# Optimization experiments

Hardware: AMD Instinct MI355X
Metric: run time of the kernel (lower is better)

The kernel has to match this reference:

```python
import jax, jax.numpy as jnp
import numpy as np

B, T, K, H, HID, OUT = 128, 128, 8, 3, 256, 2
LOG_STD_MIN, LOG_STD_MAX = -20.0, 2.0


def setup_inputs() -> dict:
    key = jax.random.key(0)
    ks = jax.random.split(key, 12)
    def lin(k, fan_in, fan_out, scale=0.05):
        return jax.random.normal(k, (fan_in, fan_out), dtype=jnp.float32) * scale
    return {
        "state": jax.random.normal(ks[0], (B, T, K), dtype=jnp.float32),
        "noise": jax.random.normal(ks[1], (B, T, OUT), dtype=jnp.float32),
        "Wq": lin(ks[2], K, H * K),
        "Wk": lin(ks[3], K, H * K),
        "Wv": lin(ks[4], K, H * K),
        "W1": lin(ks[5], H * K + K, HID),
        "b1": jnp.zeros((HID,), jnp.float32),
        "W2": lin(ks[6], HID, HID),
        "b2": jnp.zeros((HID,), jnp.float32),
        "Wmu": jax.random.uniform(ks[7], (HID, OUT), jnp.float32, -0.003, 0.003),
        "bmu": jax.random.uniform(ks[8], (OUT,), jnp.float32, -0.003, 0.003),
        "Wls": jax.random.uniform(ks[9], (HID, OUT), jnp.float32, -0.003, 0.003),
        "bls": jax.random.uniform(ks[10], (OUT,), jnp.float32, -0.003, 0.003),
    }


def reference(state, noise, Wq, Wk, Wv, W1, b1, W2, b2, Wmu, bmu, Wls, bls):
    b, t, k = state.shape
    h = H
    # off-diagonal gather indices: idx[i, m] = m if m < i else m + 1  (j != i, ascending)
    cols = jnp.arange(t - 1)
    idx = cols[None, :] + (cols[None, :] >= jnp.arange(t)[:, None]).astype(jnp.int32)  # [t, t-1]
    # rel_state[b, i, m] = state[b, idx[i, m]] - state[b, i]   -> [b, t, t-1, k]
    rel = state[:, idx, :] - state[:, :, None, :]
    # per-head projections (no bias)
    q = (state @ Wq).reshape(b, t, h, k)                      # [b, t, h, k]
    keys = (rel @ Wk).reshape(b, t, t - 1, h, k)              # [b, t, t-1, h, k]
    vals = (rel @ Wv).reshape(b, t, t - 1, h, k)
    # each query attends over its own t-1 relative keys
    scores = jnp.einsum("bthk,btmhk->bhtm", q, keys) / jnp.sqrt(jnp.float32(k))
    w = jax.nn.softmax(scores, axis=-1)                       # [b, h, t, t-1]
    x = jnp.einsum("bhtm,btmhk->bthk", w, vals).reshape(b, t, h * k)
    x = jnp.concatenate([x, state], axis=-1)                  # [b, t, h*k + k]
    x = jax.nn.relu(x @ W1 + b1)
    x = jax.nn.relu(x @ W2 + b2)
    mu = jnp.tanh(x @ Wmu + bmu)
    log_std = jnp.tanh(x @ Wls + bls)
    log_std = LOG_STD_MIN + 0.5 * (LOG_STD_MAX - LOG_STD_MIN) * (log_std + 1.0)
    std = jnp.exp(log_std)
    z = mu + std * noise                                      # rsample
    action = jnp.tanh(z)
    half_log_2pi = jnp.float32(0.5 * np.log(2.0 * np.pi))
    normal_lp = -0.5 * noise * noise - log_std - half_log_2pi
    log_prob = normal_lp - jnp.log(1.0 - action * action + 1e-7)
    log_prob = jnp.sum(log_prob, axis=-1, keepdims=True)
    return action, log_prob
```

## Files before the change

### kernel.cpp

```cpp
#include <hip/hip_runtime.h>
#include <math.h>

namespace {
constexpr int B_  = 128;
constexpr int T_  = 128;
constexpr int K_  = 8;
constexpr int H_  = 3;
constexpr int HK_ = 24;
constexpr int HID_ = 256;
constexpr int OUT_ = 2;
constexpr int PBS_ = 144;
}

typedef __attribute__((ext_vector_type(8))) short bf16x8;
typedef __attribute__((ext_vector_type(4))) float f32x4;

__device__ inline unsigned short f2bf(float x) {
    unsigned int u = __float_as_uint(x);
    u += 0x7FFFu + ((u >> 16) & 1u);
    return (unsigned short)(u >> 16);
}
__device__ inline float bf2f(unsigned short v) { return __uint_as_float((unsigned)v << 16); }

template <int CTRL>
__device__ inline float dpp_add(float v) {
    int t = __builtin_amdgcn_update_dpp(0, __float_as_int(v), CTRL, 0xF, 0xF, true);
    return v + __int_as_float(t);
}
__device__ inline float red16(float v) {
    v = dpp_add<0xB1>(v);
    v = dpp_add<0x4E>(v);
    v = dpp_add<0x141>(v);
    return dpp_add<0x140>(v);
}

__global__ __launch_bounds__(256) void prep_kernel(
    const float* __restrict__ W1, const float* __restrict__ W2,
    unsigned short* __restrict__ w1t, unsigned short* __restrict__ w2t)
{
    const int n = threadIdx.x;
    unsigned short tmp[8];
    if (blockIdx.x < 32) {
        const int k0 = blockIdx.x * 8;
        #pragma unroll
        for (int i = 0; i < 8; ++i) tmp[i] = f2bf(W2[(size_t)(k0+i)*HID_ + n]);
        *(bf16x8*)(w2t + (size_t)n*256 + k0) = *(const bf16x8*)tmp;
    } else {
        const int k0 = (blockIdx.x - 32) * 8;
        #pragma unroll
        for (int i = 0; i < 8; ++i) tmp[i] = f2bf(W1[(size_t)(k0+i)*HID_ + n]);
        *(bf16x8*)(w1t + (size_t)n*32 + k0) = *(const bf16x8*)tmp;
    }
}

__global__ __launch_bounds__(256) void fused_actor_kernel(
    const float* __restrict__ state,
    const float* __restrict__ noise,
    const float* __restrict__ Wq, const float* __restrict__ Wk,
    const float* __restrict__ Wv,
    const unsigned short* __restrict__ w1t, const float* __restrict__ b1,
    const unsigned short* __restrict__ w2t, const float* __restrict__ b2,
    const float* __restrict__ Wmu, const float* __restrict__ bmu,
    const float* __restrict__ Wls, const float* __restrict__ bls,
    float* __restrict__ out)
{
    __shared__ float wq_s[K_*HK_], wk_s[K_*HK_], wv_s[K_*HK_];
    __shared__ alignas(16) unsigned short Qb[32][HK_];
    __shared__ alignas(16) unsigned short Kb[H_][T_][8];
    __shared__ alignas(16) unsigned short Vt[H_][K_][T_];
    __shared__ alignas(16) float lsum[4][H_][32];
    __shared__ alignas(16) unsigned short a0b[32][40];
    __shared__ union alignas(16) {
        unsigned short Pb[H_][32][PBS_];
        unsigned short x1s[32][264];
    } u;
    __shared__ alignas(16) float hp[4][32][4];

    const int tid  = threadIdx.x;
    const int b    = blockIdx.x >> 2;
    const int iq   = blockIdx.x & 3;
    const int i0   = iq * 32;
    const int w    = tid >> 6;
    const int lq   = (tid >> 4) & 3;
    const int ln   = tid & 15;
    const float* sb = state + (size_t)b*T_*K_;

    if (tid < K_*HK_) { wq_s[tid]=Wq[tid]; wk_s[tid]=Wk[tid]; wv_s[tid]=Wv[tid]; }
    __syncthreads();

    {
        const int j = tid >> 1, p = tid & 1;
        const float4 s0 = *(const float4*)(sb + j*8);
        const float4 s1 = *(const float4*)(sb + j*8 + 4);
        const float sv[8] = {s0.x,s0.y,s0.z,s0.w,s1.x,s1.y,s1.z,s1.w};
        const float* ws = p ? wv_s : wk_s;
        #pragma unroll
        for (int h = 0; h < H_; ++h) {
            unsigned short pk[8];
            #pragma unroll
            for (int k = 0; k < 8; ++k) {
                const int col = h*8 + k;
                float a = 0.f;
                #pragma unroll
                for (int m = 0; m < K_; ++m) a = fmaf(sv[m], ws[m*HK_+col], a);
                pk[k] = f2bf(a);
            }
            if (p == 0) {
                *(bf16x8*)&Kb[h][j][0] = *(const bf16x8*)pk;
            } else {
                #pragma unroll
                for (int d = 0; d < 8; ++d) Vt[h][d][j] = pk[d];
            }
        }
        if (p == 0 && j >= i0 && j < i0 + 32) {
            unsigned short sb16[8];
            #pragma unroll
            for (int k = 0; k < 8; ++k) sb16[k] = f2bf(sv[k]);
            *(bf16x8*)&a0b[j - i0][HK_] = *(const bf16x8*)sb16;
        }
    }
    {
        const int il = tid >> 3;
        const int c0 = (tid & 7) * 3;
        const float4 s0 = *(const float4*)(sb + (i0+il)*8);
        const float4 s1 = *(const float4*)(sb + (i0+il)*8 + 4);
        const float sv[8] = {s0.x,s0.y,s0.z,s0.w,s1.x,s1.y,s1.z,s1.w};
        #pragma unroll
        for (int cc = 0; cc < 3; ++cc) {
            const int col = c0 + cc;
            float aq = 0.f;
            #pragma unroll
            for (int m = 0; m < K_; ++m) aq = fmaf(sv[m], wq_s[m*HK_+col], aq);
            Qb[il][col] = f2bf(aq * 0.35355339059327373f);
        }
    }
    __syncthreads();

    {
        const bf16x8 zf = {0,0,0,0,0,0,0,0};
        const f32x4 c0v = {0.f,0.f,0.f,0.f};
        float esum[H_][2][4];
        #pragma unroll
        for (int h = 0; h < H_; ++h)
            #pragma unroll
            for (int mt = 0; mt < 2; ++mt)
                #pragma unroll
                for (int r = 0; r < 4; ++r) esum[h][mt][r] = 0.f;
        #pragma unroll
        for (int h = 0; h < H_; ++h) {
            bf16x8 qa[2];
            #pragma unroll
            for (int mt = 0; mt < 2; ++mt) {
                const bf16x8 t = *(const bf16x8*)&Qb[mt*16 + ln][h*8];
                qa[mt] = (lq == 0) ? t : zf;
            }
            #pragma unroll
            for (int nti = 0; nti < 2; ++nti) {
                const int nt = w*2 + nti;
                const bf16x8 tb = *(const bf16x8*)&Kb[h][nt*16 + ln][0];
                const bf16x8 kf = (lq == 0) ? tb : zf;
                #pragma unroll
                for (int mt = 0; mt < 2; ++mt) {
                    f32x4 s = __builtin_amdgcn_mfma_f32_16x16x32_bf16(qa[mt], kf, c0v, 0,0,0);
                    #pragma unroll
                    for (int r = 0; r < 4; ++r) {
                        const int il = mt*16 + lq*4 + r;
                        const int j  = nt*16 + ln;
                        const float e = (j == i0 + il) ? 0.f : __expf(s[r]);
                        esum[h][mt][r] += e;
                        u.Pb[h][il][j] = f2bf(e);
                    }
                }
            }
        }
        #pragma unroll
        for (int h = 0; h < H_; ++h)
            #pragma unroll
            for (int mt = 0; mt < 2; ++mt)
                #pragma unroll
                for (int r = 0; r < 4; ++r) {
                    const float v = red16(esum[h][mt][r]);
                    if (ln == 0) lsum[w][h][mt*16 + lq*4 + r] = v;
                }
    }
    __syncthreads();

    {
        const bf16x8 zf = {0,0,0,0,0,0,0,0};
        for (int id = w; id < 6; id += 4) {
            const int h = id >> 1, mt = id & 1;
            f32x4 x = {0.f,0.f,0.f,0.f};
            #pragma unroll
            for (int ks = 0; ks < 4; ++ks) {
                const int k0 = ks*32;
                const bf16x8 pa = *(const bf16x8*)&u.Pb[h][mt*16 + ln][k0 + lq*8];
                const bf16x8 tv = *(const bf16x8*)&Vt[h][ln & 7][k0 + lq*8];
                const bf16x8 vf = (ln < 8) ? tv : zf;
                x = __builtin_amdgcn_mfma_f32_16x16x32_bf16(pa, vf, x, 0, 0, 0);
            }
            if (ln < 8) {
                #pragma unroll
                for (int r = 0; r < 4; ++r) {
                    const int il = mt*16 + lq*4 + r;
                    const float l = lsum[0][h][il] + lsum[1][h][il]
                                  + lsum[2][h][il] + lsum[3][h][il];
                    const float xatt = x[r] / l - bf2f(Vt[h][ln][i0 + il]);
                    a0b[il][h*8 + ln] = f2bf(xatt);
                }
            }
        }
    }
    __syncthreads();

    {
        const bf16x8 a0 = *(const bf16x8*)&a0b[ln][lq*8];
        const bf16x8 a1 = *(const bf16x8*)&a0b[16+ln][lq*8];
        #pragma unroll
        for (int nt = 0; nt < 4; ++nt) {
            const int n0 = (w*4 + nt)*16;
            const bf16x8 bf = *(const bf16x8*)(w1t + (size_t)(n0+ln)*32 + lq*8);
            const float bias = b1[n0+ln];
            f32x4 c = {bias, bias, bias, bias};
            f32x4 d0 = __builtin_amdgcn_mfma_f32_16x16x32_bf16(a0, bf, c, 0, 0, 0);
            f32x4 d1 = __builtin_amdgcn_mfma_f32_16x16x32_bf16(a1, bf, c, 0, 0, 0);
            #pragma unroll
            for (int r = 0; r < 4; ++r) {
                u.x1s[lq*4 + r][n0+ln]      = f2bf(fmaxf(d0[r], 0.f));
                u.x1s[16 + lq*4 + r][n0+ln] = f2bf(fmaxf(d1[r], 0.f));
            }
        }
    }
    __syncthreads();

    f32x4 acc2[2][4];
    #pragma unroll
    for (int nt = 0; nt < 4; ++nt) {
        const float bias = b2[(w*4+nt)*16 + ln];
        f32x4 c = {bias, bias, bias, bias};
        acc2[0][nt] = c; acc2[1][nt] = c;
    }
    #pragma unroll 2
    for (int ks = 0; ks < 8; ++ks) {
        const int k0 = ks*32;
        const bf16x8 a0 = *(const bf16x8*)&u.x1s[ln][k0 + lq*8];
        const bf16x8 a1 = *(const bf16x8*)&u.x1s[16+ln][k0 + lq*8];
        #pragma unroll
        for (int nt = 0; nt < 4; ++nt) {
            const bf16x8 bf = *(const bf16x8*)(w2t + (size_t)((w*4+nt)*16+ln)*256 + k0 + lq*8);
            acc2[0][nt] = __builtin_amdgcn_mfma_f32_16x16x32_bf16(a0, bf, acc2[0][nt], 0,0,0);
            acc2[1][nt] = __builtin_amdgcn_mfma_f32_16x16x32_bf16(a1, bf, acc2[1][nt], 0,0,0);
        }
    }

    {
        float p[2][4][4];
        #pragma unroll
        for (int mt = 0; mt < 2; ++mt)
            #pragma unroll
            for (int r = 0; r < 4; ++r)
                #pragma unroll
                for (int o = 0; o < 4; ++o) p[mt][r][o] = 0.f;
        #pragma unroll
        for (int nt = 0; nt < 4; ++nt) {
            const int n = (w*4+nt)*16 + ln;
            const float2 wm = *(const float2*)(Wmu + n*OUT_);
            const float2 wl = *(const float2*)(Wls + n*OUT_);
            #pragma unroll
            for (int mt = 0; mt < 2; ++mt) {
                #pragma unroll
                for (int r = 0; r < 4; ++r) {
                    const float x2 = fmaxf(acc2[mt][nt][r], 0.f);
                    p[mt][r][0] = fmaf(x2, wm.x, p[mt][r][0]);
                    p[mt][r][1] = fmaf(x2, wm.y, p[mt][r][1]);
                    p[mt][r][2] = fmaf(x2, wl.x, p[mt][r][2]);
                    p[mt][r][3] = fmaf(x2, wl.y, p[mt][r][3]);
                }
            }
        }
        #pragma unroll
        for (int mt = 0; mt < 2; ++mt)
            #pragma unroll
            for (int r = 0; r < 4; ++r)
                #pragma unroll
                for (int o = 0; o < 4; ++o)
                    p[mt][r][o] = red16(p[mt][r][o]);
        if (ln == 0) {
            #pragma unroll
            for (int mt = 0; mt < 2; ++mt)
                #pragma unroll
                for (int r = 0; r < 4; ++r) {
                    f32x4 pv = {p[mt][r][0], p[mt][r][1], p[mt][r][2], p[mt][r][3]};
                    *(f32x4*)&hp[w][mt*16 + lq*4 + r][0] = pv;
                }
        }
    }
    __syncthreads();

    if (tid < 32) {
        const int r = tid;
        const int grow = b*T_ + i0 + r;
        float pre[4];
        #pragma unroll
        for (int o = 0; o < 4; ++o)
            pre[o] = hp[0][r][o] + hp[1][r][o] + hp[2][r][o] + hp[3][r][o];
        float lp = 0.f;
        #pragma unroll
        for (int o = 0; o < OUT_; ++o) {
            float mu  = tanhf(pre[o]   + bmu[o]);
            float lsp = tanhf(pre[2+o] + bls[o]);
            float log_std = -20.f + 11.f * (lsp + 1.f);
            float sd = __expf(log_std);
            float n  = noise[(size_t)grow*OUT_ + o];
            float z  = fmaf(sd, n, mu);
            float a  = tanhf(z);
            out[(size_t)grow*OUT_ + o] = a;
            lp += -0.5f*n*n - log_std - 0.91893853320467274f
                  - logf(1.f - a*a + 1e-7f);
        }
        out[(size_t)B_*T_*OUT_ + grow] = lp;
    }
}

extern "C" void kernel_launch(void* const* d_in, const int* in_sizes, int n_in,
                              void* d_out, int out_size, void* d_ws, size_t ws_size,
                              hipStream_t stream)
{
    const float* state = (const float*)d_in[0];
    const float* noise = (const float*)d_in[1];
    const float* Wq  = (const float*)d_in[2];
    const float* Wk  = (const float*)d_in[3];
    const float* Wv  = (const float*)d_in[4];
    const float* W1  = (const float*)d_in[5];
    const float* b1  = (const float*)d_in[6];
    const float* W2  = (const float*)d_in[7];
    const float* b2  = (const float*)d_in[8];
    const float* Wmu = (const float*)d_in[9];
    const float* bmu = (const float*)d_in[10];
    const float* Wls = (const float*)d_in[11];
    const float* bls = (const float*)d_in[12];
    float* out = (float*)d_out;

    unsigned short* w1t = (unsigned short*)d_ws;
    unsigned short* w2t = w1t + 8192;

    prep_kernel<<<dim3(36), dim3(256), 0, stream>>>(W1, W2, w1t, w2t);
    fused_actor_kernel<<<dim3(B_*4), dim3(256), 0, stream>>>(
        state, noise, Wq, Wk, Wv, w1t, b1, w2t, b2, Wmu, bmu, Wls, bls, out);
}
```

Baseline: 95.66 us.

## Halve query rows per block to launch twice as many blocks

Each block now handles 16 query rows instead of 32, so the grid grows from 512 to 1024 blocks and all per-block tiles shrink to one MFMA row tile. The aim is more parallelism across the GPU's compute units and lower per-block latency. The cost is that each block still recomputes the full K/V projections for all 128 keys and reloads W1/W2 fragments, so that redundant work doubles. The attention-times-V stage now runs on only three of the four waves.

Result: slower. 102.9 us (+7.6%).

```diff
diff --git a/kernel.cpp b/kernel.cpp
--- a/kernel.cpp
+++ b/kernel.cpp
@@ -9,7 +9,7 @@
 constexpr int HK_ = 24;
 constexpr int HID_ = 256;
 constexpr int OUT_ = 2;
-constexpr int PBS_ = 144;
+constexpr int PBS_ = 136;
 }
 
 typedef __attribute__((ext_vector_type(8))) short bf16x8;
@@ -65,21 +65,21 @@
     float* __restrict__ out)
 {
     __shared__ float wq_s[K_*HK_], wk_s[K_*HK_], wv_s[K_*HK_];
-    __shared__ alignas(16) unsigned short Qb[32][HK_];
+    __shared__ alignas(16) unsigned short Qb[16][HK_];
     __shared__ alignas(16) unsigned short Kb[H_][T_][8];
     __shared__ alignas(16) unsigned short Vt[H_][K_][T_];
-    __shared__ alignas(16) float lsum[4][H_][32];
-    __shared__ alignas(16) unsigned short a0b[32][40];
+    __shared__ alignas(16) float lsum[4][H_][16];
+    __shared__ alignas(16) unsigned short a0b[16][40];
     __shared__ union alignas(16) {
-        unsigned short Pb[H_][32][PBS_];
-        unsigned short x1s[32][264];
+        unsigned short Pb[H_][16][PBS_];
+        unsigned short x1s[16][264];
     } u;
-    __shared__ alignas(16) float hp[4][32][4];
+    __shared__ alignas(16) float hp[4][16][4];
 
     const int tid  = threadIdx.x;
-    const int b    = blockIdx.x >> 2;
-    const int iq   = blockIdx.x & 3;
-    const int i0   = iq * 32;
+    const int b    = blockIdx.x >> 3;
+    const int iq   = blockIdx.x & 7;
+    const int i0   = iq * 16;
     const int w    = tid >> 6;
     const int lq   = (tid >> 4) & 3;
     const int ln   = tid & 15;
@@ -112,14 +112,14 @@
                 for (int d = 0; d < 8; ++d) Vt[h][d][j] = pk[d];
             }
         }
-        if (p == 0 && j >= i0 && j < i0 + 32) {
+        if (p == 0 && j >= i0 && j < i0 + 16) {
             unsigned short sb16[8];
             #pragma unroll
             for (int k = 0; k < 8; ++k) sb16[k] = f2bf(sv[k]);
             *(bf16x8*)&a0b[j - i0][HK_] = *(const bf16x8*)sb16;
         }
     }
-    {
+    if (tid < 128) {
         const int il = tid >> 3;
         const int c0 = (tid & 7) * 3;
         const float4 s0 = *(const float4*)(sb + (i0+il)*8);
@@ -139,74 +139,61 @@
     {
         const bf16x8 zf = {0,0,0,0,0,0,0,0};
         const f32x4 c0v = {0.f,0.f,0.f,0.f};
-        float esum[H_][2][4];
+        float esum[H_][4];
         #pragma unroll
         for (int h = 0; h < H_; ++h)
             #pragma unroll
-            for (int mt = 0; mt < 2; ++mt)
-                #pragma unroll
-                for (int r = 0; r < 4; ++r) esum[h][mt][r] = 0.f;
+            for (int r = 0; r < 4; ++r) esum[h][r] = 0.f;
         #pragma unroll
         for (int h = 0; h < H_; ++h) {
-            bf16x8 qa[2];
-            #pragma unroll
-            for (int mt = 0; mt < 2; ++mt) {
-                const bf16x8 t = *(const bf16x8*)&Qb[mt*16 + ln][h*8];
-                qa[mt] = (lq == 0) ? t : zf;
-            }
+            const bf16x8 tq = *(const bf16x8*)&Qb[ln][h*8];
+            const bf16x8 qa = (lq == 0) ? tq : zf;
             #pragma unroll
             for (int nti = 0; nti < 2; ++nti) {
                 const int nt = w*2 + nti;
                 const bf16x8 tb = *(const bf16x8*)&Kb[h][nt*16 + ln][0];
                 const bf16x8 kf = (lq == 0) ? tb : zf;
-                #pragma unroll
-                for (int mt = 0; mt < 2; ++mt) {
-                    f32x4 s = __builtin_amdgcn_mfma_f32_16x16x32_bf16(qa[mt], kf, c0v, 0,0,0);
-                    #pragma unroll
-                    for (int r = 0; r < 4; ++r) {
-                        const int il = mt*16 + lq*4 + r;
-                        const int j  = nt*16 + ln;
-                        const float e = (j == i0 + il) ? 0.f : __expf(s[r]);
-                        esum[h][mt][r] += e;
-                        u.Pb[h][il][j] = f2bf(e);
-                    }
-                }
-            }
-        }
-        #pragma unroll
-        for (int h = 0; h < H_; ++h)
-            #pragma unroll
-            for (int mt = 0; mt < 2; ++mt)
+                f32x4 s = __builtin_amdgcn_mfma_f32_16x16x32_bf16(qa, kf, c0v, 0,0,0);
                 #pragma unroll
                 for (int r = 0; r < 4; ++r) {
-                    const float v = red16(esum[h][mt][r]);
-                    if (ln == 0) lsum[w][h][mt*16 + lq*4 + r] = v;
+                    const int il = lq*4 + r;
+                    const int j  = nt*16 + ln;
+                    const float e = (j == i0 + il) ? 0.f : __expf(s[r]);
+                    esum[h][r] += e;
+                    u.Pb[h][il][j] = f2bf(e);
                 }
-    }
-    __syncthreads();
-
-    {
+            }
+        }
+        #pragma unroll
+        for (int h = 0; h < H_; ++h)
+            #pragma unroll
+            for (int r = 0; r < 4; ++r) {
+                const float v = red16(esum[h][r]);
+                if (ln == 0) lsum[w][h][lq*4 + r] = v;
+            }
+    }
+    __syncthreads();
+
+    if (w < H_) {
         const bf16x8 zf = {0,0,0,0,0,0,0,0};
-        for (int id = w; id < 6; id += 4) {
-            const int h = id >> 1, mt = id & 1;
-            f32x4 x = {0.f,0.f,0.f,0.f};
-            #pragma unroll
-            for (int ks = 0; ks < 4; ++ks) {
-                const int k0 = ks*32;
-                const bf16x8 pa = *(const bf16x8*)&u.Pb[h][mt*16 + ln][k0 + lq*8];
-                const bf16x8 tv = *(const bf16x8*)&Vt[h][ln & 7][k0 + lq*8];
-                const bf16x8 vf = (ln < 8) ? tv : zf;
-                x = __builtin_amdgcn_mfma_f32_16x16x32_bf16(pa, vf, x, 0, 0, 0);
-            }
-            if (ln < 8) {
-                #pragma unroll
-                for (int r = 0; r < 4; ++r) {
-                    const int il = mt*16 + lq*4 + r;
-                    const float l = lsum[0][h][il] + lsum[1][h][il]
-                                  + lsum[2][h][il] + lsum[3][h][il];
-                    const float xatt = x[r] / l - bf2f(Vt[h][ln][i0 + il]);
-                    a0b[il][h*8 + ln] = f2bf(xatt);
-                }
+        const int h = w;
+        f32x4 x = {0.f,0.f,0.f,0.f};
+        #pragma unroll
+        for (int ks = 0; ks < 4; ++ks) {
+            const int k0 = ks*32;
+            const bf16x8 pa = *(const bf16x8*)&u.Pb[h][ln][k0 + lq*8];
+            const bf16x8 tv = *(const bf16x8*)&Vt[h][ln & 7][k0 + lq*8];
+            const bf16x8 vf = (ln < 8) ? tv : zf;
+            x = __builtin_amdgcn_mfma_f32_16x16x32_bf16(pa, vf, x, 0, 0, 0);
+        }
+        if (ln < 8) {
+            #pragma unroll
+            for (int r = 0; r < 4; ++r) {
+                const int il = lq*4 + r;
+                const float l = lsum[0][h][il] + lsum[1][h][il]
+                              + lsum[2][h][il] + lsum[3][h][il];
+                const float xatt = x[r] / l - bf2f(Vt[h][ln][i0 + il]);
+                a0b[il][h*8 + ln] = f2bf(xatt);
             }
         }
     }
@@ -214,89 +201,74 @@
 
     {
         const bf16x8 a0 = *(const bf16x8*)&a0b[ln][lq*8];
-        const bf16x8 a1 = *(const bf16x8*)&a0b[16+ln][lq*8];
         #pragma unroll
         for (int nt = 0; nt < 4; ++nt) {
             const int n0 = (w*4 + nt)*16;
             const bf16x8 bf = *(const bf16x8*)(w1t + (size_t)(n0+ln)*32 + lq*8);
             const float bias = b1[n0+ln];
             f32x4 c = {bias, bias, bias, bias};
-            f32x4 d0 = __builtin_amdgcn_mfma_f32_16x16x32_bf16(a0, bf, c, 0, 0, 0);
-            f32x4 d1 = __builtin_amdgcn_mfma_f32_16x16x32_bf16(a1, bf, c, 0, 0, 0);
-            #pragma unroll
-            for (int r = 0; r < 4; ++r) {
-                u.x1s[lq*4 + r][n0+ln]      = f2bf(fmaxf(d0[r], 0.f));
-                u.x1s[16 + lq*4 + r][n0+ln] = f2bf(fmaxf(d1[r], 0.f));
-            }
-        }
-    }
-    __syncthreads();
-
-    f32x4 acc2[2][4];
+            f32x4 d = __builtin_amdgcn_mfma_f32_16x16x32_bf16(a0, bf, c, 0, 0, 0);
+            #pragma unroll
+            for (int r = 0; r < 4; ++r)
+                u.x1s[lq*4 + r][n0+ln] = f2bf(fmaxf(d[r], 0.f));
+        }
+    }
+    __syncthreads();
+
+    f32x4 acc2[4];
     #pragma unroll
     for (int nt = 0; nt < 4; ++nt) {
         const float bias = b2[(w*4+nt)*16 + ln];
         f32x4 c = {bias, bias, bias, bias};
-        acc2[0][nt] = c; acc2[1][nt] = c;
+        acc2[nt] = c;
     }
     #pragma unroll 2
     for (int ks = 0; ks < 8; ++ks) {
         const int k0 = ks*32;
         const bf16x8 a0 = *(const bf16x8*)&u.x1s[ln][k0 + lq*8];
-        const bf16x8 a1 = *(const bf16x8*)&u.x1s[16+ln][k0 + lq*8];
         #pragma unroll
         for (int nt = 0; nt < 4; ++nt) {
             const bf16x8 bf = *(const bf16x8*)(w2t + (size_t)((w*4+nt)*16+ln)*256 + k0 + lq*8);
-            acc2[0][nt] = __builtin_amdgcn_mfma_f32_16x16x32_bf16(a0, bf, acc2[0][nt], 0,0,0);
-            acc2[1][nt] = __builtin_amdgcn_mfma_f32_16x16x32_bf16(a1, bf, acc2[1][nt], 0,0,0);
+            acc2[nt] = __builtin_amdgcn_mfma_f32_16x16x32_bf16(a0, bf, acc2[nt], 0, 0, 0);
         }
     }
 
     {
-        float p[2][4][4];
-        #pragma unroll
-        for (int mt = 0; mt < 2; ++mt)
-            #pragma unroll
-            for (int r = 0; r < 4; ++r)
-                #pragma unroll
-                for (int o = 0; o < 4; ++o) p[mt][r][o] = 0.f;
+        float p[4][4];
+        #pragma unroll
+        for (int r = 0; r < 4; ++r)
+            #pragma unroll
+            for (int o = 0; o < 4; ++o) p[r][o] = 0.f;
         #pragma unroll
         for (int nt = 0; nt < 4; ++nt) {
             const int n = (w*4+nt)*16 + ln;
             const float2 wm = *(const float2*)(Wmu + n*OUT_);
             const float2 wl = *(const float2*)(Wls + n*OUT_);
             #pragma unroll
-            for (int mt = 0; mt < 2; ++mt) {
-                #pragma unroll
-                for (int r = 0; r < 4; ++r) {
-                    const float x2 = fmaxf(acc2[mt][nt][r], 0.f);
-                    p[mt][r][0] = fmaf(x2, wm.x, p[mt][r][0]);
-                    p[mt][r][1] = fmaf(x2, wm.y, p[mt][r][1]);
-                    p[mt][r][2] = fmaf(x2, wl.x, p[mt][r][2]);
-                    p[mt][r][3] = fmaf(x2, wl.y, p[mt][r][3]);
-                }
-            }
-        }
-        #pragma unroll
-        for (int mt = 0; mt < 2; ++mt)
-            #pragma unroll
-            for (int r = 0; r < 4; ++r)
-                #pragma unroll
-                for (int o = 0; o < 4; ++o)
-                    p[mt][r][o] = red16(p[mt][r][o]);
+            for (int r = 0; r < 4; ++r) {
+                const float x2 = fmaxf(acc2[nt][r], 0.f);
+                p[r][0] = fmaf(x2, wm.x, p[r][0]);
+                p[r][1] = fmaf(x2, wm.y, p[r][1]);
+                p[r][2] = fmaf(x2, wl.x, p[r][2]);
+                p[r][3] = fmaf(x2, wl.y, p[r][3]);
+            }
+        }
+        #pragma unroll
+        for (int r = 0; r < 4; ++r)
+            #pragma unroll
+            for (int o = 0; o < 4; ++o)
+                p[r][o] = red16(p[r][o]);
         if (ln == 0) {
             #pragma unroll
-            for (int mt = 0; mt < 2; ++mt)
-                #pragma unroll
-                for (int r = 0; r < 4; ++r) {
-                    f32x4 pv = {p[mt][r][0], p[mt][r][1], p[mt][r][2], p[mt][r][3]};
-                    *(f32x4*)&hp[w][mt*16 + lq*4 + r][0] = pv;
-                }
-        }
-    }
-    __syncthreads();
-
-    if (tid < 32) {
+            for (int r = 0; r < 4; ++r) {
+                f32x4 pv = {p[r][0], p[r][1], p[r][2], p[r][3]};
+                *(f32x4*)&hp[w][lq*4 + r][0] = pv;
+            }
+        }
+    }
+    __syncthreads();
+
+    if (tid < 16) {
         const int r = tid;
         const int grow = b*T_ + i0 + r;
         float pre[4];
@@ -344,6 +316,6 @@
     unsigned short* w2t = w1t + 8192;
 
     prep_kernel<<<dim3(36), dim3(256), 0, stream>>>(W1, W2, w1t, w2t);
-    fused_actor_kernel<<<dim3(B_*4), dim3(256), 0, stream>>>(
+    fused_actor_kernel<<<dim3(B_*8), dim3(256), 0, stream>>>(
         state, noise, Wq, Wk, Wv, w1t, b1, w2t, b2, Wmu, bmu, Wls, bls, out);
 }
```
